# Performance work log

Hardware: AMD Instinct MI355X
Metric: run time of the kernel (lower is better)

Reference implementation:

```python
import jax, jax.numpy as jnp
import numpy as np

N_NODES = 100000
N_EDGES = 1600000
IN_F = 128
HID_F = 128
OUT_F = 128

def _glorot(key, shape):
    lim = np.sqrt(6.0 / (shape[0] + shape[1]))
    return jax.random.uniform(key, shape, jnp.float32, -lim, lim)

def setup_inputs() -> dict:
    key = jax.random.key(0)
    ks = jax.random.split(key, 9)
    x = jax.random.normal(ks[0], (N_NODES, IN_F), jnp.float32)
    src = jax.random.randint(ks[1], (N_EDGES,), 0, N_NODES, jnp.int32)
    dst = jax.random.randint(ks[2], (N_EDGES,), 0, N_NODES, jnp.int32)
    return {
        'x': x, 'src': src, 'dst': dst,
        'W_self1': _glorot(ks[3], (IN_F, HID_F)),
        'W_neigh1': _glorot(ks[4], (IN_F, HID_F)),
        'b1': jnp.zeros((HID_F,), jnp.float32),
        'W_self2': _glorot(ks[5], (HID_F, OUT_F)),
        'W_neigh2': _glorot(ks[6], (HID_F, OUT_F)),
        'b2': jnp.zeros((OUT_F,), jnp.float32),
    }

def _sage_mean(h, src, dst, W_self, W_neigh, b, n_nodes):
    # mean-aggregate src features onto dst (DGL SAGEConv 'mean')
    msg_sum = jax.ops.segment_sum(h[src], dst, num_segments=n_nodes)  # [N, d]
    deg = jax.ops.segment_sum(jnp.ones_like(dst, jnp.float32), dst, num_segments=n_nodes)
    h_neigh = msg_sum / jnp.maximum(deg, 1.0)[:, None]
    return h @ W_self + h_neigh @ W_neigh + b

def reference(x, src, dst, W_self1, W_neigh1, b1, W_self2, W_neigh2, b2):
    n = x.shape[0]
    h = _sage_mean(x, src, dst, W_self1, W_neigh1, b1, n)
    h = _sage_mean(h, src, dst, W_self2, W_neigh2, b2, n)
    # edge-wise dot product score between endpoint features (u_dot_v)
    s = jnp.sum(h[src] * h[dst], axis=-1)  # [E]
    smin, smax = jnp.min(s), jnp.max(s)
    return (s - smin) / (smax - smin)
```

## Files before the change

kernel.cpp:

```cpp
#include <hip/hip_runtime.h>
#include <hip/hip_bf16.h>

#define F 128

typedef unsigned int uint;
typedef unsigned short ushort;
typedef __attribute__((ext_vector_type(8))) short short8;
typedef __attribute__((ext_vector_type(4))) float f32x4;

__device__ inline ushort f2bf(float f) {
    uint u = __float_as_uint(f);
    u += 0x7FFF + ((u >> 16) & 1);
    return (ushort)(u >> 16);
}
__device__ inline float2 bf2f(uint u) {
    return make_float2(__uint_as_float(u << 16), __uint_as_float(u & 0xFFFF0000u));
}

__global__ __launch_bounds__(256) void rank_kernel(const int* __restrict__ dst,
                                                   int* __restrict__ cnt,
                                                   ushort* __restrict__ rel, int E) {
    int e = blockIdx.x * 256 + threadIdx.x;
    if (e < E) rel[e] = (ushort)atomicAdd(&cnt[dst[e]], 1);
}

__global__ __launch_bounds__(256) void scan_block(const int* __restrict__ cnt,
                                                  int* __restrict__ off,
                                                  int* __restrict__ bsum, int N) {
    __shared__ int t[256];
    int i = blockIdx.x * 256 + threadIdx.x;
    int v = (i < N) ? cnt[i] : 0;
    t[threadIdx.x] = v;
    __syncthreads();
    for (int o = 1; o < 256; o <<= 1) {
        int x = (threadIdx.x >= o) ? t[threadIdx.x - o] : 0;
        __syncthreads();
        t[threadIdx.x] += x;
        __syncthreads();
    }
    if (i < N) off[i] = t[threadIdx.x] - v;
    if (threadIdx.x == 255) bsum[blockIdx.x] = t[255];
}

__global__ __launch_bounds__(512) void scan_sums(int* __restrict__ bsum, int nb) {
    __shared__ int t[512];
    int v = (threadIdx.x < nb) ? bsum[threadIdx.x] : 0;
    t[threadIdx.x] = v;
    __syncthreads();
    for (int o = 1; o < 512; o <<= 1) {
        int x = (threadIdx.x >= o) ? t[threadIdx.x - o] : 0;
        __syncthreads();
        t[threadIdx.x] += x;
        __syncthreads();
    }
    if (threadIdx.x < nb) bsum[threadIdx.x] = t[threadIdx.x] - v;
}

__global__ __launch_bounds__(256) void scan_add_rdeg(int* __restrict__ off,
                                                     const int* __restrict__ bsum,
                                                     const int* __restrict__ cnt,
                                                     float* __restrict__ rdeg, int N) {
    int i = blockIdx.x * 256 + threadIdx.x;
    if (i >= N) return;
    off[i] += bsum[blockIdx.x];
    rdeg[i] = 1.0f / fmaxf((float)cnt[i], 1.0f);
}

__global__ __launch_bounds__(256) void fill_kernel(const int* __restrict__ src,
                                                   const int* __restrict__ dst,
                                                   const int* __restrict__ off,
                                                   const ushort* __restrict__ rel,
                                                   int* __restrict__ srcS, int E) {
    int e = blockIdx.x * 256 + threadIdx.x;
    if (e >= E) return;
    srcS[off[dst[e]] + (int)rel[e]] = src[e];
}

__global__ __launch_bounds__(256) void prep_kernel(const float* __restrict__ x,
                                                   const float* __restrict__ W0,
                                                   const float* __restrict__ W1,
                                                   const float* __restrict__ W2,
                                                   const float* __restrict__ W3,
                                                   uint* __restrict__ xb,
                                                   ushort* __restrict__ Wt, int NF4) {
    int i = blockIdx.x * 256 + threadIdx.x;
    if (i < NF4) {
        float4 v = ((const float4*)x)[i];
        uint ua = (uint)f2bf(v.x) | ((uint)f2bf(v.y) << 16);
        uint ub = (uint)f2bf(v.z) | ((uint)f2bf(v.w) << 16);
        ((uint2*)xb)[i] = make_uint2(ua, ub);
    } else {
        int idx = i - NF4;
        if (idx >= 4 * 16384) return;
        int mat = idx >> 14;
        int pos = idx & 16383;
        int k = pos >> 7, n = pos & 127;
        const float* W = (mat == 0) ? W0 : (mat == 1) ? W1 : (mat == 2) ? W2 : W3;
        Wt[mat * 16384 + n * 128 + k] = f2bf(W[k * 128 + n]);
    }
}

__global__ __launch_bounds__(256) void agg_gather(const uint* __restrict__ hb,
                                                  const int* __restrict__ off,
                                                  const int* __restrict__ srcS,
                                                  const float* __restrict__ rdeg,
                                                  uint* __restrict__ msgb, int N, int E) {
    int node = blockIdx.x * 4 + (threadIdx.x >> 6);
    int lane = threadIdx.x & 63;
    if (node >= N) return;
    int p = off[node];
    int pe = (node == N - 1) ? E : off[node + 1];
    float2 acc = make_float2(0.f, 0.f);
    if (p < pe) {
        int deg = pe - p;
        int last = pe - 1;
        for (; p < pe; p += 8) {
            int i0 = min(p + 0, last), i1 = min(p + 1, last);
            int i2 = min(p + 2, last), i3 = min(p + 3, last);
            int i4 = min(p + 4, last), i5 = min(p + 5, last);
            int i6 = min(p + 6, last), i7 = min(p + 7, last);
            int s0 = srcS[i0], s1 = srcS[i1], s2 = srcS[i2], s3 = srcS[i3];
            int s4 = srcS[i4], s5 = srcS[i5], s6 = srcS[i6], s7 = srcS[i7];
            float2 f0 = bf2f(hb[(size_t)s0 * 64 + lane]);
            float2 f1 = bf2f(hb[(size_t)s1 * 64 + lane]);
            float2 f2 = bf2f(hb[(size_t)s2 * 64 + lane]);
            float2 f3 = bf2f(hb[(size_t)s3 * 64 + lane]);
            float2 f4 = bf2f(hb[(size_t)s4 * 64 + lane]);
            float2 f5 = bf2f(hb[(size_t)s5 * 64 + lane]);
            float2 f6 = bf2f(hb[(size_t)s6 * 64 + lane]);
            float2 f7 = bf2f(hb[(size_t)s7 * 64 + lane]);
            acc.x += ((f0.x + f1.x) + (f2.x + f3.x)) + ((f4.x + f5.x) + (f6.x + f7.x));
            acc.y += ((f0.y + f1.y) + (f2.y + f3.y)) + ((f4.y + f5.y) + (f6.y + f7.y));
        }
        int d = (8 - (deg & 7)) & 7;
        if (d) {
            float2 fl = bf2f(hb[(size_t)srcS[last] * 64 + lane]);
            float fd = (float)d;
            acc.x -= fd * fl.x;
            acc.y -= fd * fl.y;
        }
    }
    float rd = rdeg[node];
    msgb[(size_t)node * 64 + lane] = (uint)f2bf(acc.x * rd) | ((uint)f2bf(acc.y * rd) << 16);
}

__global__ __launch_bounds__(256) void sage_mfma(const uint* __restrict__ hb,
                                                 const uint* __restrict__ mb,
                                                 const uint* __restrict__ Wt,
                                                 const float* __restrict__ bias,
                                                 ushort* __restrict__ outb, int N) {
    int wave = threadIdx.x >> 6, lane = threadIdx.x & 63;
    int m = lane & 15, q = lane >> 4;
    int r0 = blockIdx.x * 64 + wave * 16;
    int arow = r0 + m;
    if (arow >= N) arow = N - 1;

    f32x4 acc[8];
#pragma unroll
    for (int t = 0; t < 8; t++) acc[t] = (f32x4){0.f, 0.f, 0.f, 0.f};

    const uint* hrow = hb + (size_t)arow * 64;
    const uint* mrow = mb + (size_t)arow * 64;
#pragma unroll
    for (int sel = 0; sel < 2; sel++) {
        const uint* arowp = sel ? mrow : hrow;
        const uint* wsel = Wt + sel * 8192;
#pragma unroll
        for (int kk = 0; kk < 4; kk++) {
            int ko = kk * 16 + q * 4;
            short8 a = *(const short8*)(arowp + ko);
#pragma unroll
            for (int t = 0; t < 8; t++) {
                short8 b = *(const short8*)(wsel + (size_t)(16 * t + m) * 64 + ko);
                acc[t] = __builtin_amdgcn_mfma_f32_16x16x32_bf16(a, b, acc[t], 0, 0, 0);
            }
        }
    }

#pragma unroll
    for (int t = 0; t < 8; t++) {
        float bs = bias[16 * t + m];
#pragma unroll
        for (int r = 0; r < 4; r++) {
            int orow = r0 + q * 4 + r;
            if (orow < N) outb[(size_t)orow * 128 + 16 * t + m] = f2bf(acc[t][r] + bs);
        }
    }
}

__global__ __launch_bounds__(256) void edge_score_mfma(const uint* __restrict__ hb,
                                                       const int* __restrict__ off,
                                                       const int* __restrict__ srcS,
                                                       float* __restrict__ sc,
                                                       float2* __restrict__ pmm, int N, int E) {
    int node = blockIdx.x * 4 + (threadIdx.x >> 6);
    int lane = threadIdx.x & 63;
    int m = lane & 15, q = lane >> 4;
    float lmin = INFINITY, lmax = -INFINITY;

    if (node < N) {
        int p = off[node];
        int pe = (node == N - 1) ? E : off[node + 1];
        if (p < pe) {
            const uint* nrow = hb + (size_t)node * 64;
            short8 bfr[4];
#pragma unroll
            for (int kk = 0; kk < 4; kk++)
                bfr[kk] = *(const short8*)(nrow + kk * 16 + q * 4);

            for (; p < pe; p += 16) {
                int idx = p + m;
                if (idx >= pe) idx = pe - 1;
                const uint* arow = hb + (size_t)srcS[idx] * 64;
                f32x4 acc = (f32x4){0.f, 0.f, 0.f, 0.f};
#pragma unroll
                for (int kk = 0; kk < 4; kk++) {
                    short8 a = *(const short8*)(arow + kk * 16 + q * 4);
                    acc = __builtin_amdgcn_mfma_f32_16x16x32_bf16(a, bfr[kk], acc, 0, 0, 0);
                }
                if (m == 0) {
                    if (p + 16 <= pe) {
                        *(float4*)(sc + p + q * 4) = make_float4(acc[0], acc[1], acc[2], acc[3]);
                        float mn = fminf(fminf(acc[0], acc[1]), fminf(acc[2], acc[3]));
                        float mx = fmaxf(fmaxf(acc[0], acc[1]), fmaxf(acc[2], acc[3]));
                        lmin = fminf(lmin, mn);
                        lmax = fmaxf(lmax, mx);
                    } else {
#pragma unroll
                        for (int r = 0; r < 4; r++) {
                            int e = p + q * 4 + r;
                            if (e < pe) {
                                sc[e] = acc[r];
                                lmin = fminf(lmin, acc[r]);
                                lmax = fmaxf(lmax, acc[r]);
                            }
                        }
                    }
                }
            }
        }
    }

#pragma unroll
    for (int o = 1; o <= 32; o <<= 1) {
        lmin = fminf(lmin, __shfl_xor(lmin, o));
        lmax = fmaxf(lmax, __shfl_xor(lmax, o));
    }
    __shared__ float smin[4], smax[4];
    int wv = threadIdx.x >> 6;
    if (lane == 0) { smin[wv] = lmin; smax[wv] = lmax; }
    __syncthreads();
    if (threadIdx.x == 0) {
        float mA = fminf(fminf(smin[0], smin[1]), fminf(smin[2], smin[3]));
        float MA = fmaxf(fmaxf(smax[0], smax[1]), fmaxf(smax[2], smax[3]));
        pmm[blockIdx.x] = make_float2(mA, MA);
    }
}

__global__ __launch_bounds__(1024) void minmax_final(const float2* __restrict__ pmm,
                                                     float* __restrict__ mmf, int nb) {
    float vmin = INFINITY, vmax = -INFINITY;
    for (int i = threadIdx.x; i < nb; i += 1024) {
        float2 v = pmm[i];
        vmin = fminf(vmin, v.x);
        vmax = fmaxf(vmax, v.y);
    }
#pragma unroll
    for (int o = 1; o <= 32; o <<= 1) {
        vmin = fminf(vmin, __shfl_xor(vmin, o));
        vmax = fmaxf(vmax, __shfl_xor(vmax, o));
    }
    __shared__ float smin[16], smax[16];
    int lane = threadIdx.x & 63, wv = threadIdx.x >> 6;
    if (lane == 0) { smin[wv] = vmin; smax[wv] = vmax; }
    __syncthreads();
    if (threadIdx.x == 0) {
        float m = smin[0], M = smax[0];
        for (int w = 1; w < 16; w++) { m = fminf(m, smin[w]); M = fmaxf(M, smax[w]); }
        mmf[0] = m;
        mmf[1] = M;
    }
}

__global__ __launch_bounds__(256) void norm_kernel(const float* __restrict__ sc,
                                                   const int* __restrict__ dst,
                                                   const ushort* __restrict__ rel,
                                                   const int* __restrict__ off,
                                                   float* __restrict__ out,
                                                   const float* __restrict__ mmf, int E) {
    float mn = mmf[0];
    float mx = mmf[1];
    float inv = 1.0f / (mx - mn);
    int i = blockIdx.x * 256 + threadIdx.x;
    if (i < E) {
        int p = off[dst[i]] + (int)rel[i];
        out[i] = (sc[p] - mn) * inv;
    }
}

extern "C" void kernel_launch(void* const* d_in, const int* in_sizes, int n_in,
                              void* d_out, int out_size, void* d_ws, size_t ws_size,
                              hipStream_t stream) {
    const float* x   = (const float*)d_in[0];
    const int*   src = (const int*)d_in[1];
    const int*   dst = (const int*)d_in[2];
    const float* Ws1 = (const float*)d_in[3];
    const float* Wn1 = (const float*)d_in[4];
    const float* b1  = (const float*)d_in[5];
    const float* Ws2 = (const float*)d_in[6];
    const float* Wn2 = (const float*)d_in[7];
    const float* b2  = (const float*)d_in[8];

    int N = in_sizes[0] / F;
    int E = in_sizes[1];
    float* out = (float*)d_out;

    int nbN = (N + 255) / 256;
    int nbE = (E + 255) / 256;
    int nbEdgeBlocks = (N + 3) / 4;
    int NF4 = N * F / 4;

    int* off  = (int*)d_ws;
    int* cnt  = off + N;
    int* srcS = cnt + N;
    ushort* rel = (ushort*)(srcS + E);
    float* sc = (float*)((int*)rel + E / 2);
    int* bsum = (int*)(sc + E);
    float* rdeg = (float*)(bsum + 1024);
    float* mmf = (float*)(rdeg + N);
    float2* pmm = (float2*)(mmf + 4);
    uint* Wtb = (uint*)(pmm + 25600);
    size_t elemOff = 3 * (size_t)N + 2 * (size_t)E + (size_t)E / 2 + 1024 + 4 + 51200 + 32768;
    elemOff = (elemOff + 3) & ~(size_t)3;
    uint* xb   = (uint*)d_ws + elemOff;
    uint* msgb = xb + (size_t)N * 64;
    uint* h1b  = msgb + (size_t)N * 64;
    uint* h2b  = h1b + (size_t)N * 64;

    hipMemsetAsync(cnt, 0, (size_t)N * sizeof(int), stream);

    rank_kernel<<<nbE, 256, 0, stream>>>(dst, cnt, rel, E);
    scan_block<<<nbN, 256, 0, stream>>>(cnt, off, bsum, N);
    scan_sums<<<1, 512, 0, stream>>>(bsum, nbN);
    scan_add_rdeg<<<nbN, 256, 0, stream>>>(off, bsum, cnt, rdeg, N);
    fill_kernel<<<nbE, 256, 0, stream>>>(src, dst, off, rel, srcS, E);

    prep_kernel<<<(NF4 + 4 * 16384 + 255) / 256, 256, 0, stream>>>(
        x, Ws1, Wn1, Ws2, Wn2, xb, (ushort*)Wtb, NF4);

    agg_gather<<<(N + 3) / 4, 256, 0, stream>>>(xb, off, srcS, rdeg, msgb, N, E);
    sage_mfma<<<(N + 63) / 64, 256, 0, stream>>>(xb, msgb, Wtb, b1, (ushort*)h1b, N);

    agg_gather<<<(N + 3) / 4, 256, 0, stream>>>(h1b, off, srcS, rdeg, msgb, N, E);
    sage_mfma<<<(N + 63) / 64, 256, 0, stream>>>(h1b, msgb, Wtb + 16384, b2, (ushort*)h2b, N);

    edge_score_mfma<<<nbEdgeBlocks, 256, 0, stream>>>(h2b, off, srcS, sc, pmm, N, E);
    minmax_final<<<1, 1024, 0, stream>>>(pmm, mmf, nbEdgeBlocks);
    norm_kernel<<<(E + 255) / 256, 256, 0, stream>>>(sc, dst, rel, off, out, mmf, E);
}
```

Before: 616.6 us.

## Store node features in column-chunked layout for cache-local gather aggregation

```diff
diff --git a/kernel.cpp b/kernel.cpp
--- a/kernel.cpp
+++ b/kernel.cpp
@@ -82,13 +82,18 @@
                                                    const float* __restrict__ W2,
                                                    const float* __restrict__ W3,
                                                    uint* __restrict__ xb,
-                                                   ushort* __restrict__ Wt, int NF4) {
+                                                   ushort* __restrict__ Wt, int NF4, int N) {
     int i = blockIdx.x * 256 + threadIdx.x;
     if (i < NF4) {
         float4 v = ((const float4*)x)[i];
         uint ua = (uint)f2bf(v.x) | ((uint)f2bf(v.y) << 16);
         uint ub = (uint)f2bf(v.z) | ((uint)f2bf(v.w) << 16);
-        ((uint2*)xb)[i] = make_uint2(ua, ub);
+        int r = i >> 5;
+        int g = i & 31;
+        int c = g >> 2;
+        int o = (g & 3) * 2;
+        uint* dstp = xb + (size_t)c * (size_t)N * 8 + (size_t)r * 8 + o;
+        *(uint2*)dstp = make_uint2(ua, ub);
     } else {
         int idx = i - NF4;
         if (idx >= 4 * 16384) return;
@@ -100,55 +105,55 @@
     }
 }
 
-__global__ __launch_bounds__(256) void agg_gather(const uint* __restrict__ hb,
-                                                  const int* __restrict__ off,
-                                                  const int* __restrict__ srcS,
-                                                  const float* __restrict__ rdeg,
-                                                  uint* __restrict__ msgb, int N, int E) {
-    int node = blockIdx.x * 4 + (threadIdx.x >> 6);
+__global__ __launch_bounds__(256) void agg_gather_cm(const uint* __restrict__ hb,
+                                                     const int* __restrict__ off,
+                                                     const int* __restrict__ srcS,
+                                                     const float* __restrict__ rdeg,
+                                                     uint* __restrict__ msgb,
+                                                     int N, int E) {
+    int chunk = blockIdx.x & 7;
+    int ngrp = blockIdx.x >> 3;
     int lane = threadIdx.x & 63;
+    int sub = lane >> 3;
+    int u = lane & 7;
+    int node = ngrp * 32 + (threadIdx.x >> 6) * 8 + sub;
     if (node >= N) return;
+    const uint* hc = hb + (size_t)chunk * (size_t)N * 8;
     int p = off[node];
     int pe = (node == N - 1) ? E : off[node + 1];
     float2 acc = make_float2(0.f, 0.f);
     if (p < pe) {
         int deg = pe - p;
         int last = pe - 1;
-        for (; p < pe; p += 8) {
-            int i0 = min(p + 0, last), i1 = min(p + 1, last);
-            int i2 = min(p + 2, last), i3 = min(p + 3, last);
-            int i4 = min(p + 4, last), i5 = min(p + 5, last);
-            int i6 = min(p + 6, last), i7 = min(p + 7, last);
-            int s0 = srcS[i0], s1 = srcS[i1], s2 = srcS[i2], s3 = srcS[i3];
-            int s4 = srcS[i4], s5 = srcS[i5], s6 = srcS[i6], s7 = srcS[i7];
-            float2 f0 = bf2f(hb[(size_t)s0 * 64 + lane]);
-            float2 f1 = bf2f(hb[(size_t)s1 * 64 + lane]);
-            float2 f2 = bf2f(hb[(size_t)s2 * 64 + lane]);
-            float2 f3 = bf2f(hb[(size_t)s3 * 64 + lane]);
-            float2 f4 = bf2f(hb[(size_t)s4 * 64 + lane]);
-            float2 f5 = bf2f(hb[(size_t)s5 * 64 + lane]);
-            float2 f6 = bf2f(hb[(size_t)s6 * 64 + lane]);
-            float2 f7 = bf2f(hb[(size_t)s7 * 64 + lane]);
-            acc.x += ((f0.x + f1.x) + (f2.x + f3.x)) + ((f4.x + f5.x) + (f6.x + f7.x));
-            acc.y += ((f0.y + f1.y) + (f2.y + f3.y)) + ((f4.y + f5.y) + (f6.y + f7.y));
-        }
-        int d = (8 - (deg & 7)) & 7;
+        for (; p < pe; p += 4) {
+            int i1 = min(p + 1, last), i2 = min(p + 2, last), i3 = min(p + 3, last);
+            int s0 = srcS[p], s1 = srcS[i1], s2 = srcS[i2], s3 = srcS[i3];
+            float2 f0 = bf2f(hc[(size_t)s0 * 8 + u]);
+            float2 f1 = bf2f(hc[(size_t)s1 * 8 + u]);
+            float2 f2 = bf2f(hc[(size_t)s2 * 8 + u]);
+            float2 f3 = bf2f(hc[(size_t)s3 * 8 + u]);
+            acc.x += (f0.x + f1.x) + (f2.x + f3.x);
+            acc.y += (f0.y + f1.y) + (f2.y + f3.y);
+        }
+        int d = (4 - (deg & 3)) & 3;
         if (d) {
-            float2 fl = bf2f(hb[(size_t)srcS[last] * 64 + lane]);
+            float2 fl = bf2f(hc[(size_t)srcS[last] * 8 + u]);
             float fd = (float)d;
             acc.x -= fd * fl.x;
             acc.y -= fd * fl.y;
         }
     }
     float rd = rdeg[node];
-    msgb[(size_t)node * 64 + lane] = (uint)f2bf(acc.x * rd) | ((uint)f2bf(acc.y * rd) << 16);
-}
-
-__global__ __launch_bounds__(256) void sage_mfma(const uint* __restrict__ hb,
-                                                 const uint* __restrict__ mb,
-                                                 const uint* __restrict__ Wt,
-                                                 const float* __restrict__ bias,
-                                                 ushort* __restrict__ outb, int N) {
+    msgb[(size_t)chunk * (size_t)N * 8 + (size_t)node * 8 + u] =
+        (uint)f2bf(acc.x * rd) | ((uint)f2bf(acc.y * rd) << 16);
+}
+
+template <int OUT_CM>
+__global__ __launch_bounds__(256) void sage_mfma_t(const uint* __restrict__ hb,
+                                                   const uint* __restrict__ mb,
+                                                   const uint* __restrict__ Wt,
+                                                   const float* __restrict__ bias,
+                                                   ushort* __restrict__ outb, int N) {
     int wave = threadIdx.x >> 6, lane = threadIdx.x & 63;
     int m = lane & 15, q = lane >> 4;
     int r0 = blockIdx.x * 64 + wave * 16;
@@ -159,16 +164,15 @@
 #pragma unroll
     for (int t = 0; t < 8; t++) acc[t] = (f32x4){0.f, 0.f, 0.f, 0.f};
 
-    const uint* hrow = hb + (size_t)arow * 64;
-    const uint* mrow = mb + (size_t)arow * 64;
+    size_t N8 = (size_t)N * 8;
 #pragma unroll
     for (int sel = 0; sel < 2; sel++) {
-        const uint* arowp = sel ? mrow : hrow;
+        const uint* arowp = (sel ? mb : hb) + (size_t)arow * 8 + (q & 1) * 4;
         const uint* wsel = Wt + sel * 8192;
 #pragma unroll
         for (int kk = 0; kk < 4; kk++) {
+            short8 a = *(const short8*)(arowp + (size_t)(kk * 2 + (q >> 1)) * N8);
             int ko = kk * 16 + q * 4;
-            short8 a = *(const short8*)(arowp + ko);
 #pragma unroll
             for (int t = 0; t < 8; t++) {
                 short8 b = *(const short8*)(wsel + (size_t)(16 * t + m) * 64 + ko);
@@ -183,7 +187,13 @@
 #pragma unroll
         for (int r = 0; r < 4; r++) {
             int orow = r0 + q * 4 + r;
-            if (orow < N) outb[(size_t)orow * 128 + 16 * t + m] = f2bf(acc[t][r] + bs);
+            if (orow < N) {
+                ushort val = f2bf(acc[t][r] + bs);
+                if (OUT_CM)
+                    outb[(size_t)t * (size_t)N * 16 + (size_t)orow * 16 + m] = val;
+                else
+                    outb[(size_t)orow * 128 + 16 * t + m] = val;
+            }
         }
     }
 }
@@ -346,13 +356,15 @@
     fill_kernel<<<nbE, 256, 0, stream>>>(src, dst, off, rel, srcS, E);
 
     prep_kernel<<<(NF4 + 4 * 16384 + 255) / 256, 256, 0, stream>>>(
-        x, Ws1, Wn1, Ws2, Wn2, xb, (ushort*)Wtb, NF4);
-
-    agg_gather<<<(N + 3) / 4, 256, 0, stream>>>(xb, off, srcS, rdeg, msgb, N, E);
-    sage_mfma<<<(N + 63) / 64, 256, 0, stream>>>(xb, msgb, Wtb, b1, (ushort*)h1b, N);
-
-    agg_gather<<<(N + 3) / 4, 256, 0, stream>>>(h1b, off, srcS, rdeg, msgb, N, E);
-    sage_mfma<<<(N + 63) / 64, 256, 0, stream>>>(h1b, msgb, Wtb + 16384, b2, (ushort*)h2b, N);
+        x, Ws1, Wn1, Ws2, Wn2, xb, (ushort*)Wtb, NF4, N);
+
+    int nbAgg = 8 * ((N + 31) / 32);
+
+    agg_gather_cm<<<nbAgg, 256, 0, stream>>>(xb, off, srcS, rdeg, msgb, N, E);
+    sage_mfma_t<1><<<(N + 63) / 64, 256, 0, stream>>>(xb, msgb, Wtb, b1, (ushort*)h1b, N);
+
+    agg_gather_cm<<<nbAgg, 256, 0, stream>>>(h1b, off, srcS, rdeg, msgb, N, E);
+    sage_mfma_t<0><<<(N + 63) / 64, 256, 0, stream>>>(h1b, msgb, Wtb + 16384, b2, (ushort*)h2b, N);
 
     edge_score_mfma<<<nbEdgeBlocks, 256, 0, stream>>>(h2b, off, srcS, sc, pmm, N, E);
     minmax_final<<<1, 1024, 0, stream>>>(pmm, mmf, nbEdgeBlocks);
```

New measurement: 641.4 us. +4.0%, slower.
